# Kernel tuning notes

Measured on AMD Instinct MI355X. Metric: run time of the kernel, lower is better.

## Reference

```python
import jax, jax.numpy as jnp
import numpy as np

N, K, D_IN, D_OUT = 50000, 32, 128, 128
TEMPERATURE = 1.0


def setup_inputs() -> dict:
    key = jax.random.key(0)
    k1, k2, k3 = jax.random.split(key, 3)
    feat = jax.random.normal(k1, (N, D_IN), dtype=jnp.float32)
    # Glorot-like scale so pairwise distances stay in a reasonable softmax range
    weight = jax.random.normal(k2, (D_IN, D_OUT), dtype=jnp.float32) / np.sqrt(D_IN)
    bias = jnp.zeros((D_OUT,), dtype=jnp.float32)
    # norm='none' -> unit edge weights; fixed-degree-k graph -> topk returns all k neighbors
    top_k_weights = jnp.ones((N, K), dtype=jnp.float32)
    top_k_idx = jax.random.randint(k3, (N, K), 0, N, dtype=jnp.int64)
    return {"feat": feat, "weight": weight, "bias": bias,
            "top_k_weights": top_k_weights, "top_k_idx": top_k_idx}


def reference(feat, weight, bias, top_k_weights, top_k_idx):
    # Linear projection (self.weight): [n, d_out]
    h = feat @ weight
    # Gather top-k neighbor embeddings: [n, k, d]
    fk = h[top_k_idx]
    mask = top_k_idx == -1                      # [n, k] missing-neighbor mask
    w = jnp.where(mask, 0.0, top_k_weights)     # zero out missing weights

    # Pairwise Euclidean distances among each node's k neighbors: [n, k, k]
    # ||a-b|| = sqrt(|a|^2 + |b|^2 - 2 a.b); avoids materializing [n,k,k,d]
    sq = jnp.sum(fk * fk, axis=-1)                          # [n, k]
    gram = jnp.einsum('nkd,nmd->nkm', fk, fk)               # [n, k, k]
    d2 = sq[:, :, None] + sq[:, None, :] - 2.0 * gram
    d2 = jnp.maximum(d2, 0.0)
    dist = jnp.sqrt(jnp.where(d2 > 0.0, d2, 1.0))
    dist = jnp.where(d2 > 0.0, dist, 0.0)                   # zero for identical pts / -1 idx
    # zero entries for missing pairs (matches partial_distance_matrix semantics)
    pair_mask = mask[:, :, None] | mask[:, None, :]
    dist = jnp.where(pair_mask, 0.0, dist)

    # Weighted sum of distances over neighbors (medoid cost): [n, k]
    dagg = jnp.einsum('nm,nkm->nk', w, dist)
    big = jnp.finfo(dist.dtype).max
    dagg = jnp.where(mask | ~jnp.isfinite(dagg), big, dagg)

    # Soft medoid weights
    r = jax.nn.softmax(-dagg / TEMPERATURE, axis=-1)
    # with_weight_correction=True
    r = r * w
    r = r / jnp.sum(r, axis=-1, keepdims=True)
    r = jnp.where(mask, 0.0, r)

    # spmm over the reliable adjacency: [n, d_out]
    out = jnp.einsum('nk,nkd->nd', r, fk)
    return out + bias
```

## Files before the change

kernel.cpp:

```cpp
#include <hip/hip_runtime.h>
#include <math.h>


typedef __attribute__((ext_vector_type(2)))  _Float16 half2v;
typedef __attribute__((ext_vector_type(4)))  _Float16 half4v;
typedef __attribute__((ext_vector_type(8)))  _Float16 half8;
typedef __attribute__((ext_vector_type(16))) float    f32x16;

#define NK   32
#define DIM  128
#define FKT_SZ 4224

__global__ __launch_bounds__(256) void prep(const float* __restrict__ W,
                                            _Float16* __restrict__ WT) {
    int t  = blockIdx.x * 256 + threadIdx.x;
    int nn = t >> 7, k = t & 127;
    WT[t] = (_Float16)W[k * 128 + nn];
}

__global__ __launch_bounds__(256) void gemm128(
    const float* __restrict__ A, const _Float16* __restrict__ WT,
    _Float16* __restrict__ Hq, int n)
{
    const int wave = threadIdx.x >> 6;
    const int lane = threadIdx.x & 63;
    const int l31  = lane & 31;
    const int hf   = lane >> 5;

    const int row  = blockIdx.x * 128 + wave * 32 + l31;
    const int rowc = row < n ? row : n - 1;

    f32x16 acc[4];
#pragma unroll
    for (int t = 0; t < 4; ++t)
#pragma unroll
        for (int i = 0; i < 16; ++i) acc[t][i] = 0.0f;

    const float* ap = A + (size_t)rowc * 128 + 8 * hf;
#pragma unroll
    for (int s = 0; s < 8; ++s) {
        float4 b0 = *reinterpret_cast<const float4*>(ap + 16 * s);
        float4 b1 = *reinterpret_cast<const float4*>(ap + 16 * s + 4);
        half8 bf;
        bf[0] = (_Float16)b0.x; bf[1] = (_Float16)b0.y;
        bf[2] = (_Float16)b0.z; bf[3] = (_Float16)b0.w;
        bf[4] = (_Float16)b1.x; bf[5] = (_Float16)b1.y;
        bf[6] = (_Float16)b1.z; bf[7] = (_Float16)b1.w;
#pragma unroll
        for (int t = 0; t < 4; ++t) {
            half8 af = *reinterpret_cast<const half8*>(
                WT + (size_t)(l31 + 32 * t) * 128 + 16 * s + 8 * hf);
            acc[t] = __builtin_amdgcn_mfma_f32_32x32x16_f16(af, bf, acc[t], 0, 0, 0);
        }
    }

    if (row < n) {
        _Float16* hp = Hq + (size_t)row * 128;
#pragma unroll
        for (int t = 0; t < 4; ++t)
#pragma unroll
            for (int g = 0; g < 4; ++g) {
                half4v hv;
#pragma unroll
                for (int q = 0; q < 4; ++q) hv[q] = (_Float16)acc[t][4 * g + q];
                *reinterpret_cast<half4v*>(hp + 32 * t + 8 * g + 4 * hf) = hv;
            }
    }
}

__global__ __launch_bounds__(128, 4) void softk(
    const _Float16* __restrict__ hq, const float* __restrict__ bias,
    const float* __restrict__ tkw, const int* __restrict__ idx,
    float* __restrict__ out, int n)
{
    __shared__ __align__(16) _Float16 fkT[2][FKT_SZ];
    __shared__ __align__(16) float    rbuf[2][NK];

    const int wave = threadIdx.x >> 6;
    const int lane = threadIdx.x & 63;
    int node = blockIdx.x * 2 + wave;
    if (node >= n) node = n - 1;

    const int l31 = lane & 31;
    const int hf  = lane >> 5;

    const int vid = idx[(size_t)node * NK + l31];
    const int mkc = (vid < 0) ? 1 : 0;
    const int idr = mkc ? 0 : vid;
    const float wc = mkc ? 0.0f : tkw[(size_t)node * NK + l31];

    const int d0 = 2 * lane;
    float2 bv = *reinterpret_cast<const float2*>(bias + d0);

    const half8* bp = reinterpret_cast<const half8*>(hq + (size_t)idr * DIM);
    half8 frag[8];
#pragma unroll
    for (int s = 0; s < 8; ++s) frag[s] = bp[2 * s + hf];

#pragma unroll
    for (int s = 0; s < 8; ++s) {
        int c = 2 * s + hf;
        *reinterpret_cast<half8*>(&fkT[wave][(c * 33 + l31) * 8]) = frag[s];
    }

    f32x16 acc;
#pragma unroll
    for (int i = 0; i < 16; ++i) acc[i] = 0.0f;
#pragma unroll
    for (int s = 0; s < 8; ++s)
        acc = __builtin_amdgcn_mfma_f32_32x32x16_f16(frag[s], frag[s], acc, 0, 0, 0);

    float sqp = 0.0f;
#pragma unroll
    for (int s = 0; s < 8; ++s) {
        const half2v* p2 = reinterpret_cast<const half2v*>(&frag[s]);
#pragma unroll
        for (int q = 0; q < 4; ++q)
            sqp = __builtin_amdgcn_fdot2(p2[q], p2[q], sqp, false);
    }
    float sq = sqp + __shfl_xor(sqp, 32, 64);

    {
        _Float16 shi = (_Float16)sq;
        _Float16 slo = (_Float16)(sq - (float)shi);
        _Float16 nh  = (_Float16)(-0.5f * (float)shi);
        _Float16 nl  = (_Float16)(-0.5f * (float)slo);
        _Float16 z   = (_Float16)0.0f, one = (_Float16)1.0f;
        half8 aext = {z, z, z, z, z, z, z, z};
        half8 bext = {z, z, z, z, z, z, z, z};
        if (hf == 0) {
            aext[0] = nh;  aext[1] = nl;  aext[2] = one; aext[3] = one;
            bext[0] = one; bext[1] = one; bext[2] = nh;  bext[3] = nl;
        }
        acc = __builtin_amdgcn_mfma_f32_32x32x16_f16(aext, bext, acc, 0, 0, 0);
    }

    const _Float16* fb = &fkT[wave][((d0 >> 3) * 33) * 8 + (d0 & 7)];
    half2v ev[NK];
#pragma unroll
    for (int k = 0; k < NK; ++k)
        ev[k] = *reinterpret_cast<const half2v*>(fb + 8 * k);

    const int pbase = (lane & 32) + ((lane & 32) >> 3);
    float pt[4] = {0.0f, 0.0f, 0.0f, 0.0f};
#pragma unroll
    for (int reg = 0; reg < 16; ++reg) {
        const int c = (reg & 3) + 8 * (reg >> 2);
        float wr = __shfl(wc, pbase + c, 64);
        float d2 = fmaxf(-(acc[reg] + acc[reg]), 0.0f);
        float ds = (d2 > 1e-4f) ? __builtin_amdgcn_sqrtf(d2) : 0.0f;
        pt[reg & 3] = fmaf(wr, ds, pt[reg & 3]);
    }
    float part = (pt[0] + pt[1]) + (pt[2] + pt[3]);
    float sA = part + __shfl_xor(part, 32, 64);
    if (mkc || !(sA < 3.4028235e38f)) sA = 3.4028235e38f;

    float x  = -sA;
    float mx = x;
#pragma unroll
    for (int o = 16; o > 0; o >>= 1) mx = fmaxf(mx, __shfl_xor(mx, o, 32));
    float t  = __expf(x - mx) * wc;
    float st = t;
#pragma unroll
    for (int o = 16; o > 0; o >>= 1) st += __shfl_xor(st, o, 32);
    float r = t * __builtin_amdgcn_rcpf(st);

    rbuf[wave][l31] = r;

    const float4* rb = reinterpret_cast<const float4*>(&rbuf[wave][0]);
    float o0 = 0.0f, o1 = 0.0f;
#pragma unroll
    for (int q = 0; q < 8; ++q) {
        float4 rv = rb[q];
        o0 = fmaf(rv.x, (float)ev[4*q+0][0], o0); o1 = fmaf(rv.x, (float)ev[4*q+0][1], o1);
        o0 = fmaf(rv.y, (float)ev[4*q+1][0], o0); o1 = fmaf(rv.y, (float)ev[4*q+1][1], o1);
        o0 = fmaf(rv.z, (float)ev[4*q+2][0], o0); o1 = fmaf(rv.z, (float)ev[4*q+2][1], o1);
        o0 = fmaf(rv.w, (float)ev[4*q+3][0], o0); o1 = fmaf(rv.w, (float)ev[4*q+3][1], o1);
    }
    float2 ov = { o0 + bv.x, o1 + bv.y };
    *reinterpret_cast<float2*>(out + (size_t)node * DIM + d0) = ov;
}

extern "C" void kernel_launch(void* const* d_in, const int* in_sizes, int n_in,
                              void* d_out, int out_size, void* d_ws, size_t ws_size,
                              hipStream_t stream) {
    const float* feat = (const float*)d_in[0];
    const float* W    = (const float*)d_in[1];
    const float* bias = (const float*)d_in[2];
    const float* tkw  = (const float*)d_in[3];
    const int*   idx  = (const int*)d_in[4];
    float* out = (float*)d_out;

    const int n = in_sizes[0] / DIM;
    _Float16* hq = (_Float16*)d_ws;
    _Float16* wt = hq + (size_t)n * DIM;

    prep<<<64, 256, 0, stream>>>(W, wt);
    gemm128<<<(n + 127) / 128, 256, 0, stream>>>(feat, wt, hq, n);
    softk<<<(n + 1) / 2, 128, 0, stream>>>(hq, bias, tkw, idx, out, n);
}
```

Measured before the change: 155.6 us.

## Make softk persistent with software-prefetched neighbor gathers; shrink gemm blocks

Result: slower. 164.1 us (+5.4%).

```diff
diff --git a/kernel.cpp b/kernel.cpp
--- a/kernel.cpp
+++ b/kernel.cpp
@@ -18,16 +18,15 @@
     WT[t] = (_Float16)W[k * 128 + nn];
 }
 
-__global__ __launch_bounds__(256) void gemm128(
+__global__ __launch_bounds__(64) void gemm128(
     const float* __restrict__ A, const _Float16* __restrict__ WT,
     _Float16* __restrict__ Hq, int n)
 {
-    const int wave = threadIdx.x >> 6;
-    const int lane = threadIdx.x & 63;
+    const int lane = threadIdx.x;
     const int l31  = lane & 31;
     const int hf   = lane >> 5;
 
-    const int row  = blockIdx.x * 128 + wave * 32 + l31;
+    const int row  = blockIdx.x * 32 + l31;
     const int rowc = row < n ? row : n - 1;
 
     f32x16 acc[4];
@@ -78,107 +77,136 @@
 
     const int wave = threadIdx.x >> 6;
     const int lane = threadIdx.x & 63;
-    int node = blockIdx.x * 2 + wave;
-    if (node >= n) node = n - 1;
-
-    const int l31 = lane & 31;
-    const int hf  = lane >> 5;
-
-    const int vid = idx[(size_t)node * NK + l31];
-    const int mkc = (vid < 0) ? 1 : 0;
-    const int idr = mkc ? 0 : vid;
-    const float wc = mkc ? 0.0f : tkw[(size_t)node * NK + l31];
+    const int l31  = lane & 31;
+    const int hf   = lane >> 5;
+    const int pbase = (lane & 32) + ((lane & 32) >> 3);
 
     const int d0 = 2 * lane;
-    float2 bv = *reinterpret_cast<const float2*>(bias + d0);
-
-    const half8* bp = reinterpret_cast<const half8*>(hq + (size_t)idr * DIM);
+    const float2 bv = *reinterpret_cast<const float2*>(bias + d0);
+    const _Float16* fb = &fkT[wave][((d0 >> 3) * 33) * 8 + (d0 & 7)];
+    const float4* rb = reinterpret_cast<const float4*>(&rbuf[wave][0]);
+
+    const int stride = gridDim.x * 2;
+    int nd = blockIdx.x * 2 + wave;
+    if (nd >= n) return;
+
+    int   vid = idx[(size_t)nd * NK + l31];
+    float tw  = tkw[(size_t)nd * NK + l31];
+    int   mkc = (vid < 0) ? 1 : 0;
+    float wc  = mkc ? 0.0f : tw;
     half8 frag[8];
-#pragma unroll
-    for (int s = 0; s < 8; ++s) frag[s] = bp[2 * s + hf];
-
-#pragma unroll
-    for (int s = 0; s < 8; ++s) {
-        int c = 2 * s + hf;
-        *reinterpret_cast<half8*>(&fkT[wave][(c * 33 + l31) * 8]) = frag[s];
-    }
-
-    f32x16 acc;
-#pragma unroll
-    for (int i = 0; i < 16; ++i) acc[i] = 0.0f;
-#pragma unroll
-    for (int s = 0; s < 8; ++s)
-        acc = __builtin_amdgcn_mfma_f32_32x32x16_f16(frag[s], frag[s], acc, 0, 0, 0);
-
-    float sqp = 0.0f;
-#pragma unroll
-    for (int s = 0; s < 8; ++s) {
-        const half2v* p2 = reinterpret_cast<const half2v*>(&frag[s]);
-#pragma unroll
-        for (int q = 0; q < 4; ++q)
-            sqp = __builtin_amdgcn_fdot2(p2[q], p2[q], sqp, false);
-    }
-    float sq = sqp + __shfl_xor(sqp, 32, 64);
-
     {
-        _Float16 shi = (_Float16)sq;
-        _Float16 slo = (_Float16)(sq - (float)shi);
-        _Float16 nh  = (_Float16)(-0.5f * (float)shi);
-        _Float16 nl  = (_Float16)(-0.5f * (float)slo);
-        _Float16 z   = (_Float16)0.0f, one = (_Float16)1.0f;
-        half8 aext = {z, z, z, z, z, z, z, z};
-        half8 bext = {z, z, z, z, z, z, z, z};
-        if (hf == 0) {
-            aext[0] = nh;  aext[1] = nl;  aext[2] = one; aext[3] = one;
-            bext[0] = one; bext[1] = one; bext[2] = nh;  bext[3] = nl;
-        }
-        acc = __builtin_amdgcn_mfma_f32_32x32x16_f16(aext, bext, acc, 0, 0, 0);
-    }
-
-    const _Float16* fb = &fkT[wave][((d0 >> 3) * 33) * 8 + (d0 & 7)];
-    half2v ev[NK];
-#pragma unroll
-    for (int k = 0; k < NK; ++k)
-        ev[k] = *reinterpret_cast<const half2v*>(fb + 8 * k);
-
-    const int pbase = (lane & 32) + ((lane & 32) >> 3);
-    float pt[4] = {0.0f, 0.0f, 0.0f, 0.0f};
-#pragma unroll
-    for (int reg = 0; reg < 16; ++reg) {
-        const int c = (reg & 3) + 8 * (reg >> 2);
-        float wr = __shfl(wc, pbase + c, 64);
-        float d2 = fmaxf(-(acc[reg] + acc[reg]), 0.0f);
-        float ds = (d2 > 1e-4f) ? __builtin_amdgcn_sqrtf(d2) : 0.0f;
-        pt[reg & 3] = fmaf(wr, ds, pt[reg & 3]);
-    }
-    float part = (pt[0] + pt[1]) + (pt[2] + pt[3]);
-    float sA = part + __shfl_xor(part, 32, 64);
-    if (mkc || !(sA < 3.4028235e38f)) sA = 3.4028235e38f;
-
-    float x  = -sA;
-    float mx = x;
-#pragma unroll
-    for (int o = 16; o > 0; o >>= 1) mx = fmaxf(mx, __shfl_xor(mx, o, 32));
-    float t  = __expf(x - mx) * wc;
-    float st = t;
-#pragma unroll
-    for (int o = 16; o > 0; o >>= 1) st += __shfl_xor(st, o, 32);
-    float r = t * __builtin_amdgcn_rcpf(st);
-
-    rbuf[wave][l31] = r;
-
-    const float4* rb = reinterpret_cast<const float4*>(&rbuf[wave][0]);
-    float o0 = 0.0f, o1 = 0.0f;
-#pragma unroll
-    for (int q = 0; q < 8; ++q) {
-        float4 rv = rb[q];
-        o0 = fmaf(rv.x, (float)ev[4*q+0][0], o0); o1 = fmaf(rv.x, (float)ev[4*q+0][1], o1);
-        o0 = fmaf(rv.y, (float)ev[4*q+1][0], o0); o1 = fmaf(rv.y, (float)ev[4*q+1][1], o1);
-        o0 = fmaf(rv.z, (float)ev[4*q+2][0], o0); o1 = fmaf(rv.z, (float)ev[4*q+2][1], o1);
-        o0 = fmaf(rv.w, (float)ev[4*q+3][0], o0); o1 = fmaf(rv.w, (float)ev[4*q+3][1], o1);
-    }
-    float2 ov = { o0 + bv.x, o1 + bv.y };
-    *reinterpret_cast<float2*>(out + (size_t)node * DIM + d0) = ov;
+        const int idr = mkc ? 0 : vid;
+        const half8* bp = reinterpret_cast<const half8*>(hq + (size_t)idr * DIM);
+#pragma unroll
+        for (int s = 0; s < 8; ++s) frag[s] = bp[2 * s + hf];
+    }
+
+    while (true) {
+        const int  ndn = nd + stride;
+        const bool hn  = ndn < n;
+
+        int vid_n = 0; float tw_n = 0.0f;
+        if (hn) {
+            vid_n = idx[(size_t)ndn * NK + l31];
+            tw_n  = tkw[(size_t)ndn * NK + l31];
+        }
+
+#pragma unroll
+        for (int s = 0; s < 8; ++s) {
+            int c = 2 * s + hf;
+            *reinterpret_cast<half8*>(&fkT[wave][(c * 33 + l31) * 8]) = frag[s];
+        }
+
+        f32x16 acc;
+#pragma unroll
+        for (int i = 0; i < 16; ++i) acc[i] = 0.0f;
+#pragma unroll
+        for (int s = 0; s < 8; ++s)
+            acc = __builtin_amdgcn_mfma_f32_32x32x16_f16(frag[s], frag[s], acc, 0, 0, 0);
+
+        float sqp = 0.0f;
+#pragma unroll
+        for (int s = 0; s < 8; ++s) {
+            const half2v* p2 = reinterpret_cast<const half2v*>(&frag[s]);
+#pragma unroll
+            for (int q = 0; q < 4; ++q)
+                sqp = __builtin_amdgcn_fdot2(p2[q], p2[q], sqp, false);
+        }
+        float sq = sqp + __shfl_xor(sqp, 32, 64);
+
+        const int   mk_n  = (vid_n < 0) ? 1 : 0;
+        half8 frag_n[8];
+        if (hn) {
+            const int idr_n = mk_n ? 0 : vid_n;
+            const half8* bpn = reinterpret_cast<const half8*>(hq + (size_t)idr_n * DIM);
+#pragma unroll
+            for (int s = 0; s < 8; ++s) frag_n[s] = bpn[2 * s + hf];
+        }
+
+        {
+            _Float16 shi = (_Float16)sq;
+            _Float16 slo = (_Float16)(sq - (float)shi);
+            _Float16 nh  = (_Float16)(-0.5f * (float)shi);
+            _Float16 nl  = (_Float16)(-0.5f * (float)slo);
+            _Float16 z   = (_Float16)0.0f, one = (_Float16)1.0f;
+            half8 aext = {z, z, z, z, z, z, z, z};
+            half8 bext = {z, z, z, z, z, z, z, z};
+            if (hf == 0) {
+                aext[0] = nh;  aext[1] = nl;  aext[2] = one; aext[3] = one;
+                bext[0] = one; bext[1] = one; bext[2] = nh;  bext[3] = nl;
+            }
+            acc = __builtin_amdgcn_mfma_f32_32x32x16_f16(aext, bext, acc, 0, 0, 0);
+        }
+
+        float pt[4] = {0.0f, 0.0f, 0.0f, 0.0f};
+#pragma unroll
+        for (int reg = 0; reg < 16; ++reg) {
+            const int c = (reg & 3) + 8 * (reg >> 2);
+            float wr = __shfl(wc, pbase + c, 64);
+            float d2 = fmaxf(-(acc[reg] + acc[reg]), 0.0f);
+            float ds = (d2 > 1e-4f) ? __builtin_amdgcn_sqrtf(d2) : 0.0f;
+            pt[reg & 3] = fmaf(wr, ds, pt[reg & 3]);
+        }
+        float part = (pt[0] + pt[1]) + (pt[2] + pt[3]);
+        float sA = part + __shfl_xor(part, 32, 64);
+        if (mkc || !(sA < 3.4028235e38f)) sA = 3.4028235e38f;
+
+        float x  = -sA;
+        float mx = x;
+#pragma unroll
+        for (int o = 16; o > 0; o >>= 1) mx = fmaxf(mx, __shfl_xor(mx, o, 32));
+        float t  = __expf(x - mx) * wc;
+        float st = t;
+#pragma unroll
+        for (int o = 16; o > 0; o >>= 1) st += __shfl_xor(st, o, 32);
+        float r = t * __builtin_amdgcn_rcpf(st);
+
+        rbuf[wave][l31] = r;
+
+        float o0 = 0.0f, o1 = 0.0f;
+#pragma unroll
+        for (int q = 0; q < 8; ++q) {
+            float4 rv = rb[q];
+            half2v h0 = *reinterpret_cast<const half2v*>(fb + 8 * (4 * q + 0));
+            half2v h1 = *reinterpret_cast<const half2v*>(fb + 8 * (4 * q + 1));
+            half2v h2 = *reinterpret_cast<const half2v*>(fb + 8 * (4 * q + 2));
+            half2v h3 = *reinterpret_cast<const half2v*>(fb + 8 * (4 * q + 3));
+            o0 = fmaf(rv.x, (float)h0[0], o0); o1 = fmaf(rv.x, (float)h0[1], o1);
+            o0 = fmaf(rv.y, (float)h1[0], o0); o1 = fmaf(rv.y, (float)h1[1], o1);
+            o0 = fmaf(rv.z, (float)h2[0], o0); o1 = fmaf(rv.z, (float)h2[1], o1);
+            o0 = fmaf(rv.w, (float)h3[0], o0); o1 = fmaf(rv.w, (float)h3[1], o1);
+        }
+        float2 ov = { o0 + bv.x, o1 + bv.y };
+        *reinterpret_cast<float2*>(out + (size_t)nd * DIM + d0) = ov;
+
+        if (!hn) break;
+        nd  = ndn;
+        mkc = mk_n;
+        wc  = mk_n ? 0.0f : tw_n;
+#pragma unroll
+        for (int s = 0; s < 8; ++s) frag[s] = frag_n[s];
+    }
 }
 
 extern "C" void kernel_launch(void* const* d_in, const int* in_sizes, int n_in,
@@ -195,7 +223,8 @@
     _Float16* hq = (_Float16*)d_ws;
     _Float16* wt = hq + (size_t)n * DIM;
 
+    const int gblocks = (n + 31) / 32;
     prep<<<64, 256, 0, stream>>>(W, wt);
-    gemm128<<<(n + 127) / 128, 256, 0, stream>>>(feat, wt, hq, n);
-    softk<<<(n + 1) / 2, 128, 0, stream>>>(hq, bias, tkw, idx, out, n);
-}
+    gemm128<<<gblocks, 64, 0, stream>>>(feat, wt, hq, n);
+    softk<<<gblocks, 128, 0, stream>>>(hq, bias, tkw, idx, out, n);
+}
```
